# Optimization experiments

Hardware: AMD Instinct MI355X
Metric: run time of the kernel (lower is better)

The kernel has to match this reference:

```python
import jax, jax.numpy as jnp
import numpy as np

B, NN, NC, H, V, K = 1024, 16, 16, 64, 100, 8
C = NN + NC
NEG = -1e9


def _ln_all(x, eps=1e-5):
    # torch.layer_norm(x, x.shape): normalize over ALL elements, no affine
    mu = x.mean()
    var = ((x - mu) ** 2).mean()
    return (x - mu) * jax.lax.rsqrt(var + eps)


def _ln_last(x, g, b, eps=1e-5):
    # nn.LayerNorm(H) with affine params
    mu = x.mean(-1, keepdims=True)
    var = ((x - mu) ** 2).mean(-1, keepdims=True)
    return (x - mu) * jax.lax.rsqrt(var + eps) * g + b


def _masked_ln(x, m, eps=1e-5):
    # x: [C,B,H], m: [C,B]; full-tensor layernorm over in-graph nodes only
    cnt = jnp.maximum(m.sum(1) * x.shape[-1], 1.0)
    mu = (x * m[..., None]).sum((1, 2)) / cnt
    d = x - mu[:, None, None]
    var = ((d * d) * m[..., None]).sum((1, 2)) / cnt
    return d * jax.lax.rsqrt(var + eps)[:, None, None]


def _forward(num_data, cat_data, num_w, num_b, cat_emb, fi_w1, fi_b1, fi_g, fi_be,
             fi_w2, fi_b2, gcn1_w, gcn1_b, gcn2_w, gcn2_b, pw1, pb1, pg, pbe, pw2, pb2):
    # numeric columns: Linear(1,H) per column == scalar * w + b
    fe_num = num_data[..., None] * num_w[None] + num_b[None]              # [B,NN,H]
    fe_num = _ln_all(jax.nn.relu(fe_num.reshape(B, NN * H)))
    fe_cat = cat_emb[jnp.arange(NC)[None, :], cat_data]                   # [B,NC,H]
    fe_cat = _ln_all(fe_cat.reshape(B, NC * H))
    feat = jnp.concatenate([fe_num, fe_cat], axis=1)                      # [B,C*H]
    fe3 = feat.reshape(B, C, H)
    # shared feature-importance MLP applied to every column slice (dropout = eval)
    h = _ln_last(jax.nn.relu(fe3 @ fi_w1 + fi_b1), fi_g, fi_be)
    imp = _ln_all((h @ fi_w2 + fi_b2)[..., 0])                            # [B,C]
    fe3 = fe3 * imp[..., None]
    feat = fe3.reshape(B, C * H)
    # top-K column selection per row + masked softmax
    _, idx = jax.lax.top_k(imp, K)                                        # [B,K]
    mask = jnp.zeros((B, C), jnp.float32).at[jnp.arange(B)[:, None], idx].set(1.0)
    p = jax.nn.softmax(jnp.where(mask > 0, imp, NEG), axis=1) * mask      # [B,C]
    # graph c: nodes = rows with column c in their top-K; zero column c,
    # adjacency = P P^T with zero diagonal, softmax over nonzero entries
    mT = mask.T                                                           # [C,B]
    pm = p[None, :, :] * mT[:, :, None] * (1.0 - jnp.eye(C))[:, None, :]  # [C,B,C]
    S = jnp.einsum('cik,cjk->cij', pm, pm)                                # [C,B,B]
    S = S * (1.0 - jnp.eye(B))
    pos = S > 0
    mx = jnp.max(jnp.where(pos, S, -jnp.inf), axis=(1, 2))
    mx = jnp.where(jnp.isfinite(mx), mx, 0.0)
    E = jnp.where(pos, jnp.exp(S - mx[:, None, None]), 0.0)
    Z = E.sum((1, 2))
    w = E / jnp.where(Z > 0, Z, 1.0)[:, None, None]
    # GCNConv normalization: add self-loops (weight 1) for in-graph nodes
    A = w + jnp.eye(B)[None] * mT[:, :, None]
    deg = A.sum(-1)
    dinv = jnp.where(deg > 0, jax.lax.rsqrt(deg), 0.0)
    An = dinv[:, :, None] * A * dinv[:, None, :]                          # [C,B,B]
    x = jnp.einsum('cij,jh->cih', An, feat @ gcn1_w) + gcn1_b
    x = _masked_ln(jax.nn.relu(x), mT)
    x = jnp.einsum('cij,cjh->cih', An, x @ gcn2_w) + gcn2_b
    x = _masked_ln(jax.nn.relu(x), mT)                                    # [C,B,H]
    # reassembly: each row gathers its K graph outputs, ordered by column id
    cols = jnp.sort(idx, axis=1)                                          # [B,K]
    gathered = x[cols, jnp.arange(B)[:, None]]                            # [B,K,H]
    full = jnp.concatenate([gathered, fe3], axis=1).reshape(B, (K + C) * H)
    return _ln_last(jax.nn.relu(full @ pw1 + pb1), pg, pbe) @ pw2 + pb2   # [B,2]


def setup_inputs() -> dict:
    key = jax.random.key(0)
    ks = jax.random.split(key, 12)
    s = 0.05
    f = jnp.float32
    return {
        'num_data': jax.random.normal(ks[0], (B, NN), f),
        'cat_data': jax.random.randint(ks[1], (B, NC), 0, V, jnp.int32),
        'num_w': jax.random.normal(ks[2], (NN, H), f) * s,
        'num_b': jnp.zeros((NN, H), f),
        'cat_emb': jax.random.normal(ks[3], (NC, V, H), f) * s,
        'fi_w1': jax.random.normal(ks[4], (H, H), f) * s,
        'fi_b1': jnp.zeros((H,), f),
        'fi_g': jnp.ones((H,), f),
        'fi_be': jnp.zeros((H,), f),
        'fi_w2': jax.random.normal(ks[5], (H, 1), f) * s,
        'fi_b2': jnp.zeros((1,), f),
        'gcn1_w': jax.random.normal(ks[6], (C * H, H), f) * s,
        'gcn1_b': jnp.zeros((H,), f),
        'gcn2_w': jax.random.normal(ks[7], (H, H), f) * s,
        'gcn2_b': jnp.zeros((H,), f),
        'pw1': jax.random.normal(ks[8], ((K + C) * H, H), f) * s,
        'pb1': jnp.zeros((H,), f),
        'pg': jnp.ones((H,), f),
        'pbe': jnp.zeros((H,), f),
        'pw2': jax.random.normal(ks[9], (H, 2), f) * s,
        'pb2': jnp.zeros((2,), f),
    }


def reference(num_data, cat_data, num_w, num_b, cat_emb, fi_w1, fi_b1, fi_g, fi_be,
              fi_w2, fi_b2, gcn1_w, gcn1_b, gcn2_w, gcn2_b, pw1, pb1, pg, pbe, pw2, pb2):
    return _forward(num_data, cat_data, num_w, num_b, cat_emb, fi_w1, fi_b1, fi_g, fi_be,
                    fi_w2, fi_b2, gcn1_w, gcn1_b, gcn2_w, gcn2_b, pw1, pb1, pg, pbe, pw2, pb2)
```

## Files before the change

### kernel.cpp

```cpp
#include <hip/hip_runtime.h>
#include <hip/hip_bf16.h>

#define BB   1024
#define NNUM 16
#define NCAT 16
#define HH   64
#define VV   100
#define KK   8
#define CC   32
#define CH   2048
#define FULLW 2560

#define OFF_FE3   0u
#define OFF_X1    2097152u
#define OFF_X2    4194304u
#define OFF_G     6291456u
#define OFF_SIMP  6356992u
#define OFF_P     6389760u
#define OFF_ROWE  6422528u
#define OFF_DINV  6455296u
#define OFF_F     6488064u
#define OFF_STATS 6520832u
#define OFF_Z     6520840u
#define OFF_X1S   6520872u
#define OFF_X2S   6520936u
#define OFF_COLS  6521000u
#define OFF_LIST  6529192u
#define OFF_CNT   6561960u
#define OFF_AOFF  6561992u
#define OFF_AN    6562048u

__device__ inline float wsum64(float v){
  #pragma unroll
  for (int o = 32; o; o >>= 1) v += __shfl_xor(v, o);
  return v;
}

__global__ __launch_bounds__(256) void k_init(float* ws){
  int t = threadIdx.x;
  if (t < 8)  ws[OFF_STATS + t] = 0.f;
  if (t < 64) ws[OFF_X1S + t] = 0.f;
  if (t < 64) ws[OFF_X2S + t] = 0.f;
  if (t < 32) ws[OFF_Z + t] = 0.f;
}

__global__ __launch_bounds__(256) void k_fe(const float* __restrict__ nd,
                                            const float* __restrict__ nw,
                                            const float* __restrict__ nb,
                                            const int* __restrict__ cd,
                                            const float* __restrict__ emb,
                                            float* __restrict__ ws){
  float* fe3 = ws + OFF_FE3;
  float lsn = 0.f, lssn = 0.f, lsc = 0.f, lssc = 0.f;
  int idx = blockIdx.x*256 + threadIdx.x;
  {
    int h4 = idx & 15, fn = (idx >> 4) & 15, b = (idx >> 8) & 1023;
    bool isNum = (idx < 262144);
    if (isNum){
      float s = nd[b*NNUM + fn];
      float4 w = *(const float4*)&nw[fn*HH + h4*4];
      float4 bi = *(const float4*)&nb[fn*HH + h4*4];
      float4 v;
      v.x = fmaxf(s*w.x + bi.x, 0.f);
      v.y = fmaxf(s*w.y + bi.y, 0.f);
      v.z = fmaxf(s*w.z + bi.z, 0.f);
      v.w = fmaxf(s*w.w + bi.w, 0.f);
      *(float4*)&fe3[b*CH + fn*HH + h4*4] = v;
      lsn = v.x+v.y+v.z+v.w;
      lssn = v.x*v.x+v.y*v.y+v.z*v.z+v.w*v.w;
    } else {
      int j = cd[b*NCAT + fn];
      float4 v = *(const float4*)&emb[((size_t)fn*VV + j)*HH + h4*4];
      *(float4*)&fe3[b*CH + (NNUM + fn)*HH + h4*4] = v;
      lsc = v.x+v.y+v.z+v.w;
      lssc = v.x*v.x+v.y*v.y+v.z*v.z+v.w*v.w;
    }
  }
  __shared__ float sh[16];
  lsn = wsum64(lsn); lssn = wsum64(lssn);
  lsc = wsum64(lsc); lssc = wsum64(lssc);
  int w = threadIdx.x >> 6;
  if ((threadIdx.x & 63) == 0){ sh[w] = lsn; sh[4+w] = lssn; sh[8+w] = lsc; sh[12+w] = lssc; }
  __syncthreads();
  if (threadIdx.x == 0){
    if (blockIdx.x < 1024){
      atomicAdd(ws + OFF_STATS + 0, sh[0]+sh[1]+sh[2]+sh[3]);
      atomicAdd(ws + OFF_STATS + 1, sh[4]+sh[5]+sh[6]+sh[7]);
    } else {
      atomicAdd(ws + OFF_STATS + 2, sh[8]+sh[9]+sh[10]+sh[11]);
      atomicAdd(ws + OFF_STATS + 3, sh[12]+sh[13]+sh[14]+sh[15]);
    }
  }
}

__global__ __launch_bounds__(256) void k_fi(const float* __restrict__ w1,
                                            const float* __restrict__ b1,
                                            const float* __restrict__ g,
                                            const float* __restrict__ be,
                                            const float* __restrict__ w2,
                                            const float* __restrict__ b2f,
                                            float* __restrict__ ws){
  __shared__ float w1s[64][65];
  __shared__ float xs[4][64];
  int wv = threadIdx.x >> 6, lane = threadIdx.x & 63;
  for (int q = threadIdx.x; q < 4096; q += 256) w1s[q >> 6][q & 63] = w1[q];
  __syncthreads();
  const float* fe3 = ws + OFF_FE3;
  const float* st = ws + OFF_STATS;
  const float NinvG = 1.f/1048576.f;
  float mun = st[0]*NinvG, varn = st[1]*NinvG - mun*mun;
  float rsn = rsqrtf(varn + 1e-5f);
  float muc = st[2]*NinvG, varc = st[3]*NinvG - muc*muc;
  float rsc = rsqrtf(varc + 1e-5f);
  float b1l = b1[lane], gl = g[lane], bel = be[lane], w2l = w2[lane], b2s = b2f[0];
  int gw = blockIdx.x*4 + wv;
  float ls = 0.f, lss = 0.f;
  for (int it = 0; it < 8; ++it){
    int row = gw + 4096*it;
    bool isn = (row & 31) < NNUM;
    float mu0 = isn ? mun : muc, rs0 = isn ? rsn : rsc;
    float x = (fe3[(size_t)row*64 + lane] - mu0)*rs0;
    xs[wv][lane] = x;
    float t0 = 0.f, t1 = 0.f, t2 = 0.f, t3 = 0.f;
    #pragma unroll
    for (int k = 0; k < 64; k += 4){
      float4 xq = *(const float4*)&xs[wv][k];
      t0 += xq.x*w1s[k][lane];
      t1 += xq.y*w1s[k+1][lane];
      t2 += xq.z*w1s[k+2][lane];
      t3 += xq.w*w1s[k+3][lane];
    }
    float t = (t0+t1) + (t2+t3) + b1l;
    t = fmaxf(t, 0.f);
    float mu = wsum64(t)*(1.f/64.f);
    float d = t - mu;
    float var = wsum64(d*d)*(1.f/64.f);
    float rs = rsqrtf(var + 1e-5f);
    float h1 = d*rs*gl + bel;
    float s = wsum64(h1*w2l) + b2s;
    if (lane == 0) ws[OFF_SIMP + row] = s;
    ls += s; lss += s*s;
  }
  __shared__ float sh[8];
  if (lane == 0){ sh[wv] = ls; sh[4+wv] = lss; }
  __syncthreads();
  if (threadIdx.x == 0){
    atomicAdd(ws + OFF_STATS + 4, sh[0]+sh[1]+sh[2]+sh[3]);
    atomicAdd(ws + OFF_STATS + 5, sh[4]+sh[5]+sh[6]+sh[7]);
  }
}

__global__ __launch_bounds__(256) void k_topk(float* __restrict__ ws){
  int b = blockIdx.x;
  __shared__ float imp[CC];
  if (threadIdx.x < CC){
    const float Ninv = 1.f/32768.f;
    float s4 = ws[OFF_STATS+4], s5 = ws[OFF_STATS+5];
    float mu = s4*Ninv, var = s5*Ninv - mu*mu;
    float rs = rsqrtf(var + 1e-5f);
    imp[threadIdx.x] = (ws[OFF_SIMP + b*CC + threadIdx.x] - mu)*rs;
  }
  __syncthreads();
  if (threadIdx.x == 0){
    unsigned taken = 0;
    float m0 = 0.f;
    for (int t = 0; t < KK; t++){
      float best = -1e30f; int bi = 0;
      for (int c = 0; c < CC; c++){
        if (!((taken >> c) & 1u) && imp[c] > best){ best = imp[c]; bi = c; }
      }
      taken |= 1u << bi;
      if (t == 0) m0 = best;
    }
    float sum = 0.f;
    int* cols = (int*)(ws + OFF_COLS);
    int tn = 0;
    for (int c = 0; c < CC; c++){
      if ((taken >> c) & 1u){ cols[b*KK + tn] = c; tn++; sum += expf(imp[c] - m0); }
    }
    float inv = 1.f/sum;
    for (int c = 0; c < CC; c++){
      float pv = ((taken >> c) & 1u) ? expf(imp[c] - m0)*inv : 0.f;
      ws[OFF_P + b*CC + c] = pv;
    }
  }
  __syncthreads();
  float* fe3 = ws + OFF_FE3;
  const float* st = ws + OFF_STATS;
  const float NinvG = 1.f/1048576.f;
  float mun = st[0]*NinvG, varn = st[1]*NinvG - mun*mun;
  float rsn = rsqrtf(varn + 1e-5f);
  float muc = st[2]*NinvG, varc = st[3]*NinvG - muc*muc;
  float rsc = rsqrtf(varc + 1e-5f);
  for (int q4 = threadIdx.x; q4 < 512; q4 += 256){
    int c = q4 >> 4;
    float mu, rs;
    if (c < NNUM){ mu = mun; rs = rsn; } else { mu = muc; rs = rsc; }
    float im = imp[c]*rs;
    float4 v = *(float4*)&fe3[b*CH + q4*4];
    v.x = (v.x - mu)*im; v.y = (v.y - mu)*im;
    v.z = (v.z - mu)*im; v.w = (v.w - mu)*im;
    *(float4*)&fe3[b*CH + q4*4] = v;
  }
}

__global__ __launch_bounds__(256) void k_lists(float* __restrict__ ws){
  int c = blockIdx.x;
  __shared__ int cnt_s;
  if (threadIdx.x == 0) cnt_s = 0;
  __syncthreads();
  int* list = (int*)(ws + OFF_LIST);
  for (int b = threadIdx.x; b < BB; b += 256){
    if (ws[OFF_P + b*CC + c] > 0.f){
      int slot = atomicAdd(&cnt_s, 1);
      list[c*BB + slot] = b;
    }
  }
  __syncthreads();
  if (threadIdx.x == 0) ((int*)(ws + OFF_CNT))[c] = cnt_s;
}

__global__ void k_offs(float* __restrict__ ws){
  if (threadIdx.x == 0){
    const int* cnt = (const int*)(ws + OFF_CNT);
    int* aoff = (int*)(ws + OFF_AOFF);
    int acc = 0;
    for (int c = 0; c < CC; c++){ aoff[c] = acc; acc += cnt[c]*cnt[c]; }
    aoff[CC] = acc;
  }
}

__global__ __launch_bounds__(256) void k_G(const float* __restrict__ w1g, float* __restrict__ ws){
  __shared__ float frow[4][CH];
  int wv = threadIdx.x >> 6, lane = threadIdx.x & 63;
  int b = blockIdx.x*4 + wv;
  const float* fe3 = ws + OFF_FE3;
  for (int q = 0; q < 32; q++) frow[wv][q*64 + lane] = fe3[b*CH + q*64 + lane];
  __syncthreads();
  float a0 = 0.f, a1 = 0.f, a2 = 0.f, a3 = 0.f;
  #pragma unroll 8
  for (int k = 0; k < CH; k += 4){
    float4 fq = *(const float4*)&frow[wv][k];
    a0 += fq.x*w1g[(k+0)*64 + lane];
    a1 += fq.y*w1g[(k+1)*64 + lane];
    a2 += fq.z*w1g[(k+2)*64 + lane];
    a3 += fq.w*w1g[(k+3)*64 + lane];
  }
  ws[OFF_G + b*64 + lane] = (a0+a1) + (a2+a3);
}

__global__ __launch_bounds__(256) void k_E(float* __restrict__ ws){
  int c = blockIdx.x;
  int n = ((const int*)(ws + OFF_CNT))[c];
  int r0 = blockIdx.y*32;
  if (r0 >= n) return;
  const int* list = (const int*)(ws + OFF_LIST) + c*BB;
  const float* p = ws + OFF_P;
  int base = ((const int*)(ws + OFF_AOFF))[c];
  float* An = ws + OFF_AN;
  __shared__ float pis[32][36];
  __shared__ float pT[32][72];
  int wv = threadIdx.x >> 6, lane = threadIdx.x & 63;
  for (int idx = threadIdx.x; idx < 1024; idx += 256){
    int r = idx >> 5, u = idx & 31;
    int ii = r0 + r;
    float v = 0.f;
    if (ii < n && u != c) v = p[list[ii]*CC + u];
    pis[r][u] = v;
  }
  float re[8] = {0.f,0.f,0.f,0.f,0.f,0.f,0.f,0.f};
  int rowBase = r0 + wv*8;
  for (int jt = 0; jt < n; jt += 64){
    __syncthreads();
    for (int idx = threadIdx.x; idx < 2048; idx += 256){
      int t = idx & 63, u = idx >> 6;
      int jj = jt + t;
      float v = 0.f;
      if (jj < n) v = p[list[jj]*CC + u];
      pT[u][t] = v;
    }
    __syncthreads();
    int jj = jt + lane;
    bool jok = (jj < n);
    #pragma unroll
    for (int r = 0; r < 8; r++){
      int row = rowBase + r;
      if (row < n){
        float4 pi0 = *(const float4*)&pis[wv*8 + r][0];
        float4 pi1 = *(const float4*)&pis[wv*8 + r][4];
        float4 pi2 = *(const float4*)&pis[wv*8 + r][8];
        float4 pi3 = *(const float4*)&pis[wv*8 + r][12];
        float4 pi4 = *(const float4*)&pis[wv*8 + r][16];
        float4 pi5 = *(const float4*)&pis[wv*8 + r][20];
        float4 pi6 = *(const float4*)&pis[wv*8 + r][24];
        float4 pi7 = *(const float4*)&pis[wv*8 + r][28];
        float s0 = pi0.x*pT[0][lane]  + pi1.x*pT[4][lane]  + pi2.x*pT[8][lane]  + pi3.x*pT[12][lane]
                 + pi4.x*pT[16][lane] + pi5.x*pT[20][lane] + pi6.x*pT[24][lane] + pi7.x*pT[28][lane];
        float s1 = pi0.y*pT[1][lane]  + pi1.y*pT[5][lane]  + pi2.y*pT[9][lane]  + pi3.y*pT[13][lane]
                 + pi4.y*pT[17][lane] + pi5.y*pT[21][lane] + pi6.y*pT[25][lane] + pi7.y*pT[29][lane];
        float s2 = pi0.z*pT[2][lane]  + pi1.z*pT[6][lane]  + pi2.z*pT[10][lane] + pi3.z*pT[14][lane]
                 + pi4.z*pT[18][lane] + pi5.z*pT[22][lane] + pi6.z*pT[26][lane] + pi7.z*pT[30][lane];
        float s3 = pi0.w*pT[3][lane]  + pi1.w*pT[7][lane]  + pi2.w*pT[11][lane] + pi3.w*pT[15][lane]
                 + pi4.w*pT[19][lane] + pi5.w*pT[23][lane] + pi6.w*pT[27][lane] + pi7.w*pT[31][lane];
        float S = (s0+s1) + (s2+s3);
        float Ev = 0.f;
        if (jok && jj != row && S > 0.f) Ev = __expf(S);
        if (jok) An[(size_t)base + (size_t)row*n + jj] = Ev;
        re[r] += Ev;
      }
    }
  }
  float zpart = 0.f;
  #pragma unroll
  for (int r = 0; r < 8; r++){
    float rsum = wsum64(re[r]);
    int row = rowBase + r;
    if (lane == 0 && row < n){
      ws[OFF_ROWE + c*BB + row] = rsum;
      zpart += rsum;
    }
  }
  __shared__ float sh[4];
  if (lane == 0) sh[wv] = zpart;
  __syncthreads();
  if (threadIdx.x == 0) atomicAdd(ws + OFF_Z + c, sh[0]+sh[1]+sh[2]+sh[3]);
}

__global__ __launch_bounds__(256) void k_scl(float* __restrict__ ws){
  int c = blockIdx.x;
  int n = ((const int*)(ws + OFF_CNT))[c];
  int ii = blockIdx.y*256 + threadIdx.x;
  if (ii >= n) return;
  float z = ws[OFF_Z + c];
  float zp = (z > 0.f) ? z : 1.f;
  float re = ws[OFF_ROWE + c*BB + ii];
  float di = rsqrtf(re/zp + 1.0f);
  ws[OFF_DINV + c*BB + ii] = di;
  ws[OFF_F    + c*BB + ii] = di*rsqrtf(zp);
}

__global__ __launch_bounds__(256) void k_agg(const float* __restrict__ src, int chanStride,
                                             const float* __restrict__ bias,
                                             float* __restrict__ outb,
                                             float* __restrict__ statsb,
                                             float* __restrict__ ws){
  int c = blockIdx.x;
  int n = ((const int*)(ws + OFF_CNT))[c];
  int r0 = blockIdx.y*16;
  if (r0 >= n) return;
  int base = ((const int*)(ws + OFF_AOFF))[c];
  const int* lst = (const int*)(ws + OFF_LIST) + c*BB;
  const float* E = ws + OFF_AN + (size_t)base;
  const float* fpos = ws + OFF_F + c*BB;
  const float* dpos = ws + OFF_DINV + c*BB;
  const float* srcc = src + (size_t)c*(size_t)chanStride*64;
  __shared__ float cf[16][128];
  __shared__ float sl[128][64];
  __shared__ float frow_s[16];
  int wv = threadIdx.x >> 6, lane = threadIdx.x & 63;
  if (threadIdx.x < 16){
    int rr = r0 + threadIdx.x;
    frow_s[threadIdx.x] = (rr < n) ? fpos[rr] : 0.f;
  }
  int rw = wv*4;
  float acc[4] = {0.f,0.f,0.f,0.f};
  for (int jt = 0; jt < n; jt += 128){
    __syncthreads();
    #pragma unroll
    for (int s = 0; s < 8; s++){
      int slot = threadIdx.x + s*256;
      int j = slot >> 4, q = slot & 15;
      int jj = jt + j;
      float4 v = make_float4(0.f,0.f,0.f,0.f);
      if (jj < n){
        int jg = lst[jj];
        v = *(const float4*)&srcc[(size_t)jg*64 + q*4];
      }
      *(float4*)&sl[j][q*4] = v;
    }
    #pragma unroll
    for (int s = 0; s < 8; s++){
      int idx = threadIdx.x + s*256;
      int r = idx >> 7, j = idx & 127;
      int row = r0 + r, jj = jt + j;
      float v = 0.f;
      if (row < n && jj < n){
        if (jj == row){ float d = dpos[row]; v = d*d; }
        else v = E[(size_t)row*n + jj] * fpos[jj] * frow_s[r];
      }
      cf[r][j] = v;
    }
    __syncthreads();
    int jcnt = n - jt; if (jcnt > 128) jcnt = 128;
    int jcnt4 = (jcnt + 3) & ~3;
    for (int j = 0; j < jcnt4; j += 4){
      float v0 = sl[j+0][lane];
      float v1 = sl[j+1][lane];
      float v2 = sl[j+2][lane];
      float v3 = sl[j+3][lane];
      #pragma unroll
      for (int r = 0; r < 4; r++){
        float4 c4 = *(const float4*)&cf[rw + r][j];
        acc[r] += c4.x*v0 + c4.y*v1 + c4.z*v2 + c4.w*v3;
      }
    }
  }
  float bl = bias[lane];
  float s = 0.f, ssq = 0.f;
  #pragma unroll
  for (int r = 0; r < 4; r++){
    int row = r0 + rw + r;
    if (row < n){
      float a = fmaxf(acc[r] + bl, 0.f);
      outb[((size_t)c*BB + lst[row])*64 + lane] = a;
      s += a; ssq += a*a;
    }
  }
  s = wsum64(s); ssq = wsum64(ssq);
  __shared__ float shs[4], shq[4];
  if (lane == 0){ shs[wv] = s; shq[wv] = ssq; }
  __syncthreads();
  if (threadIdx.x == 0){
    float ts = shs[0]+shs[1]+shs[2]+shs[3];
    float tq = shq[0]+shq[1]+shq[2]+shq[3];
    if (tq != 0.f){
      atomicAdd(statsb + 2*c,     ts);
      atomicAdd(statsb + 2*c + 1, tq);
    }
  }
}

__global__ __launch_bounds__(256) void k_y(const float* __restrict__ w2g, float* __restrict__ ws){
  __shared__ float w2s[64][65];
  __shared__ float xs[4][64];
  int wv = threadIdx.x >> 6, lane = threadIdx.x & 63;
  for (int q = threadIdx.x; q < 4096; q += 256) w2s[q >> 6][q & 63] = w2g[q];
  __syncthreads();
  int c = blockIdx.x;
  int n = ((const int*)(ws + OFF_CNT))[c];
  const int* list = (const int*)(ws + OFF_LIST);
  float* x1 = ws + OFF_X1;
  float cntf = fmaxf((float)(n*64), 1.f);
  float mu = ws[OFF_X1S + 2*c]/cntf;
  float var = ws[OFF_X1S + 2*c + 1]/cntf - mu*mu;
  float rs = rsqrtf(var + 1e-5f);
  for (int ii = blockIdx.y*4 + wv; ii < n; ii += 64){
    int i = list[c*BB + ii];
    size_t bse = ((size_t)c*BB + i)*64;
    float xn = (x1[bse + lane] - mu)*rs;
    xs[wv][lane] = xn;
    float y0 = 0.f, y1 = 0.f, y2 = 0.f, y3 = 0.f;
    #pragma unroll
    for (int k = 0; k < 64; k += 4){
      float4 xq = *(const float4*)&xs[wv][k];
      y0 += xq.x*w2s[k][lane];
      y1 += xq.y*w2s[k+1][lane];
      y2 += xq.z*w2s[k+2][lane];
      y3 += xq.w*w2s[k+3][lane];
    }
    x1[bse + lane] = (y0+y1) + (y2+y3);
  }
}

__global__ __launch_bounds__(256) void k_final(const float* __restrict__ pw1,
                                               const float* __restrict__ pb1,
                                               const float* __restrict__ pg,
                                               const float* __restrict__ pbe,
                                               const float* __restrict__ pw2,
                                               const float* __restrict__ pb2,
                                               float* __restrict__ ws,
                                               float* __restrict__ out){
  __shared__ float fr[4][FULLW];
  int wv = threadIdx.x >> 6, lane = threadIdx.x & 63;
  int b = blockIdx.x*4 + wv;
  const int* cols = (const int*)(ws + OFF_COLS);
  const int* cnt  = (const int*)(ws + OFF_CNT);
  const float* x2 = ws + OFF_X2;
  const float* fe3 = ws + OFF_FE3;
  #pragma unroll
  for (int t = 0; t < KK; t++){
    int ct = cols[b*KK + t];
    float cfv = fmaxf((float)(cnt[ct]*64), 1.f);
    float mu = ws[OFF_X2S + 2*ct]/cfv;
    float var = ws[OFF_X2S + 2*ct + 1]/cfv - mu*mu;
    float rs = rsqrtf(var + 1e-5f);
    fr[wv][t*64 + lane] = (x2[((size_t)ct*BB + b)*64 + lane] - mu)*rs;
  }
  #pragma unroll
  for (int q = 0; q < 32; q++) fr[wv][512 + q*64 + lane] = fe3[b*CH + q*64 + lane];
  __syncthreads();
  float a0 = 0.f, a1 = 0.f, a2 = 0.f, a3 = 0.f;
  #pragma unroll 8
  for (int k = 0; k < FULLW; k += 4){
    float4 fq = *(const float4*)&fr[wv][k];
    a0 += fq.x*pw1[(k+0)*64 + lane];
    a1 += fq.y*pw1[(k+1)*64 + lane];
    a2 += fq.z*pw1[(k+2)*64 + lane];
    a3 += fq.w*pw1[(k+3)*64 + lane];
  }
  float acc = (a0+a1) + (a2+a3) + pb1[lane];
  acc = fmaxf(acc, 0.f);
  float mu = wsum64(acc)*(1.f/64.f);
  float d = acc - mu;
  float var = wsum64(d*d)*(1.f/64.f);
  float rs = rsqrtf(var + 1e-5f);
  float zn = d*rs*pg[lane] + pbe[lane];
  float s0 = wsum64(zn*pw2[lane*2 + 0]);
  float s1 = wsum64(zn*pw2[lane*2 + 1]);
  if (lane == 0){
    out[b*2 + 0] = s0 + pb2[0];
    out[b*2 + 1] = s1 + pb2[1];
  }
}

extern "C" void kernel_launch(void* const* d_in, const int* in_sizes, int n_in,
                              void* d_out, int out_size, void* d_ws, size_t ws_size,
                              hipStream_t stream){
  (void)in_sizes; (void)n_in; (void)out_size; (void)ws_size;
  const float* num_data = (const float*)d_in[0];
  const int*   cat_data = (const int*)d_in[1];
  const float* num_w   = (const float*)d_in[2];
  const float* num_b   = (const float*)d_in[3];
  const float* cat_emb = (const float*)d_in[4];
  const float* fi_w1   = (const float*)d_in[5];
  const float* fi_b1   = (const float*)d_in[6];
  const float* fi_g    = (const float*)d_in[7];
  const float* fi_be   = (const float*)d_in[8];
  const float* fi_w2   = (const float*)d_in[9];
  const float* fi_b2   = (const float*)d_in[10];
  const float* gcn1_w  = (const float*)d_in[11];
  const float* gcn1_b  = (const float*)d_in[12];
  const float* gcn2_w  = (const float*)d_in[13];
  const float* gcn2_b  = (const float*)d_in[14];
  const float* pw1     = (const float*)d_in[15];
  const float* pb1     = (const float*)d_in[16];
  const float* pg      = (const float*)d_in[17];
  const float* pbe     = (const float*)d_in[18];
  const float* pw2     = (const float*)d_in[19];
  const float* pb2     = (const float*)d_in[20];
  float* ws  = (float*)d_ws;
  float* out = (float*)d_out;

  k_init<<<1, 256, 0, stream>>>(ws);
  k_fe<<<2048, 256, 0, stream>>>(num_data, num_w, num_b, cat_data, cat_emb, ws);
  k_fi<<<1024, 256, 0, stream>>>(fi_w1, fi_b1, fi_g, fi_be, fi_w2, fi_b2, ws);
  k_topk<<<1024, 256, 0, stream>>>(ws);
  k_lists<<<32, 256, 0, stream>>>(ws);
  k_offs<<<1, 64, 0, stream>>>(ws);
  k_G<<<256, 256, 0, stream>>>(gcn1_w, ws);
  k_E<<<dim3(32, 32), 256, 0, stream>>>(ws);
  k_scl<<<dim3(32, 4), 256, 0, stream>>>(ws);
  k_agg<<<dim3(32, 64), 256, 0, stream>>>(ws + OFF_G, 0, gcn1_b, ws + OFF_X1, ws + OFF_X1S, ws);
  k_y<<<dim3(32, 16), 256, 0, stream>>>(gcn2_w, ws);
  k_agg<<<dim3(32, 64), 256, 0, stream>>>(ws + OFF_X1, BB, gcn2_b, ws + OFF_X2, ws + OFF_X2S, ws);
  k_final<<<256, 256, 0, stream>>>(pw1, pb1, pg, pbe, pw2, pb2, ws, out);
}
```

Measured before the change: 524.8 us.

## Split column dimension across grid z in k_E and k_agg with atomic accumulation

The k_E and k_agg kernels now split the neighbour (column) dimension across a third grid axis. Each block handles one 64- or 128-wide column tile instead of looping over all tiles, and partial row sums and aggregation outputs are combined with atomicAdd. Bias, ReLU and the layer-norm statistics move into a new k_epi kernel, and a larger zeroing kernel clears X1/X2 and the row-sum buffers beforehand. The aim is more parallelism for the graph-sized loops, which were serialised per block. The cost is many more atomics, extra kernel launches, and a full memset of the 8 MB X1/X2 buffers.

```diff
diff --git a/kernel.cpp b/kernel.cpp
--- a/kernel.cpp
+++ b/kernel.cpp
@@ -36,12 +36,15 @@
   return v;
 }
 
-__global__ __launch_bounds__(256) void k_init(float* ws){
-  int t = threadIdx.x;
-  if (t < 8)  ws[OFF_STATS + t] = 0.f;
-  if (t < 64) ws[OFF_X1S + t] = 0.f;
-  if (t < 64) ws[OFF_X2S + t] = 0.f;
-  if (t < 32) ws[OFF_Z + t] = 0.f;
+__global__ __launch_bounds__(256) void k_zero(float* __restrict__ ws){
+  unsigned t = blockIdx.x*256 + threadIdx.x;
+  float4 z = make_float4(0.f,0.f,0.f,0.f);
+  if (t < 1048576u){
+    *(float4*)&ws[OFF_X1 + t*4] = z;
+  } else {
+    unsigned u = t - 1048576u;
+    if (u < 24618u) *(float4*)&ws[OFF_ROWE + u*4] = z;
+  }
 }
 
 __global__ __launch_bounds__(256) void k_fe(const float* __restrict__ nd,
@@ -253,7 +256,8 @@
   int c = blockIdx.x;
   int n = ((const int*)(ws + OFF_CNT))[c];
   int r0 = blockIdx.y*32;
-  if (r0 >= n) return;
+  int jt = blockIdx.z*64;
+  if (r0 >= n || jt >= n) return;
   const int* list = (const int*)(ws + OFF_LIST) + c*BB;
   const float* p = ws + OFF_P;
   int base = ((const int*)(ws + OFF_AOFF))[c];
@@ -268,62 +272,56 @@
     if (ii < n && u != c) v = p[list[ii]*CC + u];
     pis[r][u] = v;
   }
-  float re[8] = {0.f,0.f,0.f,0.f,0.f,0.f,0.f,0.f};
+  for (int idx = threadIdx.x; idx < 2048; idx += 256){
+    int t = idx & 63, u = idx >> 6;
+    int jj = jt + t;
+    float v = 0.f;
+    if (jj < n) v = p[list[jj]*CC + u];
+    pT[u][t] = v;
+  }
+  __syncthreads();
+  int jj = jt + lane;
+  bool jok = (jj < n);
   int rowBase = r0 + wv*8;
-  for (int jt = 0; jt < n; jt += 64){
-    __syncthreads();
-    for (int idx = threadIdx.x; idx < 2048; idx += 256){
-      int t = idx & 63, u = idx >> 6;
-      int jj = jt + t;
-      float v = 0.f;
-      if (jj < n) v = p[list[jj]*CC + u];
-      pT[u][t] = v;
-    }
-    __syncthreads();
-    int jj = jt + lane;
-    bool jok = (jj < n);
-    #pragma unroll
-    for (int r = 0; r < 8; r++){
-      int row = rowBase + r;
-      if (row < n){
-        float4 pi0 = *(const float4*)&pis[wv*8 + r][0];
-        float4 pi1 = *(const float4*)&pis[wv*8 + r][4];
-        float4 pi2 = *(const float4*)&pis[wv*8 + r][8];
-        float4 pi3 = *(const float4*)&pis[wv*8 + r][12];
-        float4 pi4 = *(const float4*)&pis[wv*8 + r][16];
-        float4 pi5 = *(const float4*)&pis[wv*8 + r][20];
-        float4 pi6 = *(const float4*)&pis[wv*8 + r][24];
-        float4 pi7 = *(const float4*)&pis[wv*8 + r][28];
-        float s0 = pi0.x*pT[0][lane]  + pi1.x*pT[4][lane]  + pi2.x*pT[8][lane]  + pi3.x*pT[12][lane]
-                 + pi4.x*pT[16][lane] + pi5.x*pT[20][lane] + pi6.x*pT[24][lane] + pi7.x*pT[28][lane];
-        float s1 = pi0.y*pT[1][lane]  + pi1.y*pT[5][lane]  + pi2.y*pT[9][lane]  + pi3.y*pT[13][lane]
-                 + pi4.y*pT[17][lane] + pi5.y*pT[21][lane] + pi6.y*pT[25][lane] + pi7.y*pT[29][lane];
-        float s2 = pi0.z*pT[2][lane]  + pi1.z*pT[6][lane]  + pi2.z*pT[10][lane] + pi3.z*pT[14][lane]
-                 + pi4.z*pT[18][lane] + pi5.z*pT[22][lane] + pi6.z*pT[26][lane] + pi7.z*pT[30][lane];
-        float s3 = pi0.w*pT[3][lane]  + pi1.w*pT[7][lane]  + pi2.w*pT[11][lane] + pi3.w*pT[15][lane]
-                 + pi4.w*pT[19][lane] + pi5.w*pT[23][lane] + pi6.w*pT[27][lane] + pi7.w*pT[31][lane];
-        float S = (s0+s1) + (s2+s3);
-        float Ev = 0.f;
-        if (jok && jj != row && S > 0.f) Ev = __expf(S);
-        if (jok) An[(size_t)base + (size_t)row*n + jj] = Ev;
-        re[r] += Ev;
+  float zpart = 0.f;
+  #pragma unroll
+  for (int r = 0; r < 8; r++){
+    int row = rowBase + r;
+    if (row < n){
+      float4 pi0 = *(const float4*)&pis[wv*8 + r][0];
+      float4 pi1 = *(const float4*)&pis[wv*8 + r][4];
+      float4 pi2 = *(const float4*)&pis[wv*8 + r][8];
+      float4 pi3 = *(const float4*)&pis[wv*8 + r][12];
+      float4 pi4 = *(const float4*)&pis[wv*8 + r][16];
+      float4 pi5 = *(const float4*)&pis[wv*8 + r][20];
+      float4 pi6 = *(const float4*)&pis[wv*8 + r][24];
+      float4 pi7 = *(const float4*)&pis[wv*8 + r][28];
+      float s0 = pi0.x*pT[0][lane]  + pi1.x*pT[4][lane]  + pi2.x*pT[8][lane]  + pi3.x*pT[12][lane]
+               + pi4.x*pT[16][lane] + pi5.x*pT[20][lane] + pi6.x*pT[24][lane] + pi7.x*pT[28][lane];
+      float s1 = pi0.y*pT[1][lane]  + pi1.y*pT[5][lane]  + pi2.y*pT[9][lane]  + pi3.y*pT[13][lane]
+               + pi4.y*pT[17][lane] + pi5.y*pT[21][lane] + pi6.y*pT[25][lane] + pi7.y*pT[29][lane];
+      float s2 = pi0.z*pT[2][lane]  + pi1.z*pT[6][lane]  + pi2.z*pT[10][lane] + pi3.z*pT[14][lane]
+               + pi4.z*pT[18][lane] + pi5.z*pT[22][lane] + pi6.z*pT[26][lane] + pi7.z*pT[30][lane];
+      float s3 = pi0.w*pT[3][lane]  + pi1.w*pT[7][lane]  + pi2.w*pT[11][lane] + pi3.w*pT[15][lane]
+               + pi4.w*pT[19][lane] + pi5.w*pT[23][lane] + pi6.w*pT[27][lane] + pi7.w*pT[31][lane];
+      float S = (s0+s1) + (s2+s3);
+      float Ev = 0.f;
+      if (jok && jj != row && S > 0.f) Ev = __expf(S);
+      if (jok) An[(size_t)base + (size_t)row*n + jj] = Ev;
+      float rsum = wsum64(Ev);
+      if (lane == 0){
+        atomicAdd(ws + OFF_ROWE + c*BB + row, rsum);
+        zpart += rsum;
       }
-    }
-  }
-  float zpart = 0.f;
-  #pragma unroll
-  for (int r = 0; r < 8; r++){
-    float rsum = wsum64(re[r]);
-    int row = rowBase + r;
-    if (lane == 0 && row < n){
-      ws[OFF_ROWE + c*BB + row] = rsum;
-      zpart += rsum;
     }
   }
   __shared__ float sh[4];
   if (lane == 0) sh[wv] = zpart;
   __syncthreads();
-  if (threadIdx.x == 0) atomicAdd(ws + OFF_Z + c, sh[0]+sh[1]+sh[2]+sh[3]);
+  if (threadIdx.x == 0){
+    float z = sh[0]+sh[1]+sh[2]+sh[3];
+    if (z != 0.f) atomicAdd(ws + OFF_Z + c, z);
+  }
 }
 
 __global__ __launch_bounds__(256) void k_scl(float* __restrict__ ws){
@@ -340,14 +338,13 @@
 }
 
 __global__ __launch_bounds__(256) void k_agg(const float* __restrict__ src, int chanStride,
-                                             const float* __restrict__ bias,
                                              float* __restrict__ outb,
-                                             float* __restrict__ statsb,
                                              float* __restrict__ ws){
   int c = blockIdx.x;
   int n = ((const int*)(ws + OFF_CNT))[c];
   int r0 = blockIdx.y*16;
-  if (r0 >= n) return;
+  int jt = blockIdx.z*128;
+  if (r0 >= n || jt >= n) return;
   int base = ((const int*)(ws + OFF_AOFF))[c];
   const int* lst = (const int*)(ws + OFF_LIST) + c*BB;
   const float* E = ws + OFF_AN + (size_t)base;
@@ -362,59 +359,72 @@
     int rr = r0 + threadIdx.x;
     frow_s[threadIdx.x] = (rr < n) ? fpos[rr] : 0.f;
   }
+  #pragma unroll
+  for (int s = 0; s < 8; s++){
+    int slot = threadIdx.x + s*256;
+    int j = slot >> 4, q = slot & 15;
+    int jj = jt + j;
+    float4 v = make_float4(0.f,0.f,0.f,0.f);
+    if (jj < n){
+      int jg = lst[jj];
+      v = *(const float4*)&srcc[(size_t)jg*64 + q*4];
+    }
+    *(float4*)&sl[j][q*4] = v;
+  }
+  __syncthreads();
+  #pragma unroll
+  for (int s = 0; s < 8; s++){
+    int idx = threadIdx.x + s*256;
+    int r = idx >> 7, j = idx & 127;
+    int row = r0 + r, jj = jt + j;
+    float v = 0.f;
+    if (row < n && jj < n){
+      if (jj == row){ float d = dpos[row]; v = d*d; }
+      else v = E[(size_t)row*n + jj] * fpos[jj] * frow_s[r];
+    }
+    cf[r][j] = v;
+  }
+  __syncthreads();
   int rw = wv*4;
   float acc[4] = {0.f,0.f,0.f,0.f};
-  for (int jt = 0; jt < n; jt += 128){
-    __syncthreads();
+  int jcnt = n - jt; if (jcnt > 128) jcnt = 128;
+  int jcnt4 = (jcnt + 3) & ~3;
+  for (int j = 0; j < jcnt4; j += 4){
+    float v0 = sl[j+0][lane];
+    float v1 = sl[j+1][lane];
+    float v2 = sl[j+2][lane];
+    float v3 = sl[j+3][lane];
     #pragma unroll
-    for (int s = 0; s < 8; s++){
-      int slot = threadIdx.x + s*256;
-      int j = slot >> 4, q = slot & 15;
-      int jj = jt + j;
-      float4 v = make_float4(0.f,0.f,0.f,0.f);
-      if (jj < n){
-        int jg = lst[jj];
-        v = *(const float4*)&srcc[(size_t)jg*64 + q*4];
-      }
-      *(float4*)&sl[j][q*4] = v;
-    }
-    #pragma unroll
-    for (int s = 0; s < 8; s++){
-      int idx = threadIdx.x + s*256;
-      int r = idx >> 7, j = idx & 127;
-      int row = r0 + r, jj = jt + j;
-      float v = 0.f;
-      if (row < n && jj < n){
-        if (jj == row){ float d = dpos[row]; v = d*d; }
-        else v = E[(size_t)row*n + jj] * fpos[jj] * frow_s[r];
-      }
-      cf[r][j] = v;
-    }
-    __syncthreads();
-    int jcnt = n - jt; if (jcnt > 128) jcnt = 128;
-    int jcnt4 = (jcnt + 3) & ~3;
-    for (int j = 0; j < jcnt4; j += 4){
-      float v0 = sl[j+0][lane];
-      float v1 = sl[j+1][lane];
-      float v2 = sl[j+2][lane];
-      float v3 = sl[j+3][lane];
-      #pragma unroll
-      for (int r = 0; r < 4; r++){
-        float4 c4 = *(const float4*)&cf[rw + r][j];
-        acc[r] += c4.x*v0 + c4.y*v1 + c4.z*v2 + c4.w*v3;
-      }
-    }
-  }
-  float bl = bias[lane];
-  float s = 0.f, ssq = 0.f;
+    for (int r = 0; r < 4; r++){
+      float4 c4 = *(const float4*)&cf[rw + r][j];
+      acc[r] += c4.x*v0 + c4.y*v1 + c4.z*v2 + c4.w*v3;
+    }
+  }
   #pragma unroll
   for (int r = 0; r < 4; r++){
     int row = r0 + rw + r;
     if (row < n){
-      float a = fmaxf(acc[r] + bl, 0.f);
-      outb[((size_t)c*BB + lst[row])*64 + lane] = a;
-      s += a; ssq += a*a;
-    }
+      atomicAdd(&outb[((size_t)c*BB + lst[row])*64 + lane], acc[r]);
+    }
+  }
+}
+
+__global__ __launch_bounds__(256) void k_epi(float* __restrict__ buf,
+                                             const float* __restrict__ bias,
+                                             float* __restrict__ statsb,
+                                             float* __restrict__ ws){
+  int c = blockIdx.x;
+  int n = ((const int*)(ws + OFF_CNT))[c];
+  const int* list = (const int*)(ws + OFF_LIST);
+  int wv = threadIdx.x >> 6, lane = threadIdx.x & 63;
+  float bl = bias[lane];
+  float s = 0.f, ssq = 0.f;
+  for (int ii = blockIdx.y*4 + wv; ii < n; ii += 64){
+    int i = list[c*BB + ii];
+    size_t idx = ((size_t)c*BB + i)*64 + lane;
+    float a = fmaxf(buf[idx] + bl, 0.f);
+    buf[idx] = a;
+    s += a; ssq += a*a;
   }
   s = wsum64(s); ssq = wsum64(ssq);
   __shared__ float shs[4], shq[4];
@@ -541,17 +551,19 @@
   float* ws  = (float*)d_ws;
   float* out = (float*)d_out;
 
-  k_init<<<1, 256, 0, stream>>>(ws);
+  k_zero<<<4192, 256, 0, stream>>>(ws);
   k_fe<<<2048, 256, 0, stream>>>(num_data, num_w, num_b, cat_data, cat_emb, ws);
   k_fi<<<1024, 256, 0, stream>>>(fi_w1, fi_b1, fi_g, fi_be, fi_w2, fi_b2, ws);
   k_topk<<<1024, 256, 0, stream>>>(ws);
   k_lists<<<32, 256, 0, stream>>>(ws);
   k_offs<<<1, 64, 0, stream>>>(ws);
   k_G<<<256, 256, 0, stream>>>(gcn1_w, ws);
-  k_E<<<dim3(32, 32), 256, 0, stream>>>(ws);
+  k_E<<<dim3(32, 32, 16), 256, 0, stream>>>(ws);
   k_scl<<<dim3(32, 4), 256, 0, stream>>>(ws);
-  k_agg<<<dim3(32, 64), 256, 0, stream>>>(ws + OFF_G, 0, gcn1_b, ws + OFF_X1, ws + OFF_X1S, ws);
+  k_agg<<<dim3(32, 64, 8), 256, 0, stream>>>(ws + OFF_G, 0, ws + OFF_X1, ws);
+  k_epi<<<dim3(32, 16), 256, 0, stream>>>(ws + OFF_X1, gcn1_b, ws + OFF_X1S, ws);
   k_y<<<dim3(32, 16), 256, 0, stream>>>(gcn2_w, ws);
-  k_agg<<<dim3(32, 64), 256, 0, stream>>>(ws + OFF_X1, BB, gcn2_b, ws + OFF_X2, ws + OFF_X2S, ws);
+  k_agg<<<dim3(32, 64, 8), 256, 0, stream>>>(ws + OFF_X1, BB, ws + OFF_X2, ws);
+  k_epi<<<dim3(32, 16), 256, 0, stream>>>(ws + OFF_X2, gcn2_b, ws + OFF_X2S, ws);
   k_final<<<256, 256, 0, stream>>>(pw1, pb1, pg, pbe, pw2, pb2, ws, out);
 }
```

New measurement: 572.2 us. +9.0%, slower.
